# Kernel tuning notes

Measured on AMD Instinct MI355X. Metric: run time of the kernel, lower is better.

The kernel has to match this reference:

```python
import jax, jax.numpy as jnp
import numpy as np

B, N, H = 4, 512, 64
EDGE_IN = 2 * H + 4

def silu(x):
    return x * jax.nn.sigmoid(x)

def setup_inputs() -> dict:
    key = jax.random.key(0)
    ks = jax.random.split(key, 16)
    def w(k, fan_in, fan_out):
        return (jax.random.normal(k, (fan_in, fan_out), jnp.float32) / np.sqrt(fan_in)).astype(jnp.float32)
    return {
        "h":   jax.random.normal(ks[0], (B, N, H), jnp.float32),
        "pos": jax.random.normal(ks[1], (B, N, 2), jnp.float32),
        "vel": jax.random.normal(ks[2], (B, N, 2), jnp.float32),
        # edge_mlp: Linear(2H+4,H) SiLU Linear(H,H) SiLU
        "ew1": w(ks[3], EDGE_IN, H), "eb1": jnp.zeros((H,), jnp.float32),
        "ew2": w(ks[4], H, H),       "eb2": jnp.zeros((H,), jnp.float32),
        # force_mlp: Linear(H,H) SiLU Linear(H,1)
        "fw1": w(ks[5], H, H),       "fb1": jnp.zeros((H,), jnp.float32),
        "fw2": w(ks[6], H, 1),       "fb2": jnp.zeros((1,), jnp.float32),
        # node_mlp: Linear(2H,H) SiLU Linear(H,H)
        "nw1": w(ks[7], 2 * H, H),   "nb1": jnp.zeros((H,), jnp.float32),
        "nw2": w(ks[8], H, H),       "nb2": jnp.zeros((H,), jnp.float32),
    }

def reference(h, pos, vel, ew1, eb1, ew2, eb2, fw1, fb1, fw2, fb2, nw1, nb1, nw2, nb2):
    b, n, hd = h.shape
    # rel_pos[b,i,j] = pos[b,j] - pos[b,i]  (torch: pos.unsqueeze(1) - pos.unsqueeze(2))
    rel_pos = pos[:, None, :, :] - pos[:, :, None, :]                # (B,N,N,2)
    dist_sq = jnp.sum(rel_pos ** 2, axis=-1, keepdims=True)         # (B,N,N,1)
    dist = jnp.sqrt(dist_sq + 1e-8)
    normal = rel_pos / dist                                          # (B,N,N,2)
    speed_sq = jnp.sum(vel ** 2, axis=-1, keepdims=True)             # (B,N,1)
    rel_vel = vel[:, None, :, :] - vel[:, :, None, :]                # (B,N,N,2)
    approach = jnp.sum(rel_vel * normal, axis=-1, keepdims=True)     # (B,N,N,1)
    h_i = jnp.broadcast_to(h[:, :, None, :], (b, n, n, hd))
    h_j = jnp.broadcast_to(h[:, None, :, :], (b, n, n, hd))
    sp_i = jnp.broadcast_to(speed_sq[:, :, None, :], (b, n, n, 1))
    sp_j = jnp.broadcast_to(speed_sq[:, None, :, :], (b, n, n, 1))
    edge_feat = jnp.concatenate([h_i, h_j, dist_sq, sp_i, sp_j, approach], axis=-1)  # (B,N,N,2H+4)
    m_ij = silu(silu(edge_feat @ ew1 + eb1) @ ew2 + eb2)             # (B,N,N,H)
    force_weight = silu(m_ij @ fw1 + fb1) @ fw2 + fb2                # (B,N,N,1)
    force_ij = force_weight * normal                                 # (B,N,N,2)
    mask = (1.0 - jnp.eye(n, dtype=h.dtype))[None, :, :, None]       # zero self-edges
    force = jnp.sum(force_ij * mask, axis=2)                         # (B,N,2)
    m_agg = jnp.sum(m_ij * mask, axis=2)                             # (B,N,H)
    h_new = silu(jnp.concatenate([h, m_agg], axis=-1) @ nw1 + nb1) @ nw2 + nb2  # (B,N,H)
    return (h_new, force)
```

## Files before the change

### kernel.cpp

```cpp
#include <hip/hip_runtime.h>
#include <hip/hip_bf16.h>
#include <stdint.h>

#define NB 4
#define NN 512
#define NH 64

typedef __attribute__((ext_vector_type(4))) float f32x4;
typedef __attribute__((ext_vector_type(8))) short short8;

__device__ __forceinline__ unsigned short bf16b(float f){
  union { float f; uint32_t u; } c; c.f = f;
  uint32_t u = c.u;
  u += 0x7fffu + ((u >> 16) & 1u);
  return (unsigned short)(u >> 16);
}
__device__ __forceinline__ uint32_t pk2(float lo, float hi){
  uint32_t d;
  asm("v_cvt_pk_bf16_f32 %0, %1, %2" : "=v"(d) : "v"(lo), "v"(hi));
  return d;
}
__device__ __forceinline__ float silu(float x){
  float e = __expf(-x);
  return x * __builtin_amdgcn_rcpf(1.0f + e);
}

__launch_bounds__(256)
__global__ void k_precompute(const float* __restrict__ h,
                             const float* __restrict__ vel,
                             const float* __restrict__ ew1,
                             const float* __restrict__ eb1,
                             const float* __restrict__ ew2,
                             const float* __restrict__ fw1,
                             float* __restrict__ wa, float* __restrict__ wc,
                             unsigned short* __restrict__ wef,
                             unsigned short* __restrict__ wff){
  const int tid = threadIdx.x;
  if (blockIdx.x >= 512){
    const int idx = (blockIdx.x - 512) * 256 + tid;
    const int mat = idx >> 12;
    const int r = idx & 4095;
    const int e2 = r & 7;
    const int lane = (r >> 3) & 63;
    const int mtkk = r >> 9;
    const int kk = mtkk >> 2, mt = mtkk & 3;
    const int krow = kk*32 + (lane >> 4)*8 + e2;
    const int dr = lane & 15;
    const int col_nat  = mt*16 + dr;
    const int col_perm = 32*(mt>>1) + 8*(dr>>2) + 4*(mt&1) + (dr&3);
    if (mat) wff[r] = bf16b(fw1[krow*NH + col_nat]);
    else     wef[r] = bf16b(ew2[krow*NH + col_perm]);
    return;
  }
  const int row = blockIdx.x * 4 + (tid >> 6);
  const int t = tid & 63;
  const float* hr = h + row * NH;
  const float vx = vel[row*2], vy = vel[row*2+1];
  const float sp = vx*vx + vy*vy;
  float aa = eb1[t] + sp * ew1[129*NH + t];
  float cc =          sp * ew1[130*NH + t];
  #pragma unroll 8
  for (int k = 0; k < NH; ++k){
    float hk = hr[k];
    aa += hk * ew1[k*NH + t];
    cc += hk * ew1[(NH + k)*NH + t];
  }
  wa[row*NH + t] = aa;
  wc[row*NH + t] = cc;
}

__launch_bounds__(256)
__global__ void k_edges(const float* __restrict__ pos,
                        const float* __restrict__ vel,
                        const float* __restrict__ wa,
                        const float* __restrict__ wc,
                        const float* __restrict__ ew1,
                        const float* __restrict__ eb2,
                        const float* __restrict__ fb1,
                        const float* __restrict__ fw2,
                        const float* __restrict__ fb2,
                        const unsigned short* __restrict__ wef,
                        const unsigned short* __restrict__ wff,
                        float* __restrict__ wmagg,
                        float* __restrict__ outF){
  const int row = blockIdx.x;
  const int b = row >> 9;
  const int i = row & (NN - 1);
  const int tid = threadIdx.x;
  const int l = tid & 63;
  const int w = tid >> 6;
  const int e = l & 15;
  const int g = l >> 4;
  const int bN = b * NN;

  __shared__ alignas(16) float seb2[64];
  __shared__ alignas(16) float sfb1[64];
  __shared__ alignas(16) float sfw2[64];
  if (tid < 64){
    seb2[tid] = eb2[tid];
    sfb1[tid] = fb1[tid];
    sfw2[tid] = fw2[tid];
  }

  const float pix = pos[row*2], piy = pos[row*2+1];
  const float vix = vel[row*2], viy = vel[row*2+1];
  const float fb2s = fb2[0];

  const float* arow = wa + row * NH;
  const f32x4 af0a = *(const f32x4*)(arow + 8*g);
  const f32x4 af0b = *(const f32x4*)(arow + 8*g + 4);
  const f32x4 af1a = *(const f32x4*)(arow + 32 + 8*g);
  const f32x4 af1b = *(const f32x4*)(arow + 32 + 8*g + 4);
  const float* wD = ew1 + 128*NH;
  const f32x4 d0a = *(const f32x4*)(wD + 8*g);
  const f32x4 d0b = *(const f32x4*)(wD + 8*g + 4);
  const f32x4 d1a = *(const f32x4*)(wD + 32 + 8*g);
  const f32x4 d1b = *(const f32x4*)(wD + 32 + 8*g + 4);
  const float* wP = ew1 + 131*NH;
  const f32x4 p0a = *(const f32x4*)(wP + 8*g);
  const f32x4 p0b = *(const f32x4*)(wP + 8*g + 4);
  const f32x4 p1a = *(const f32x4*)(wP + 32 + 8*g);
  const f32x4 p1b = *(const f32x4*)(wP + 32 + 8*g + 4);

  short8 aw[2][4], fw[2][4];
  #pragma unroll
  for (int kk = 0; kk < 2; ++kk){
    #pragma unroll
    for (int mt = 0; mt < 4; ++mt){
      aw[kk][mt] = *(const short8*)(wef + ((kk*4 + mt)*64 + l)*8);
      fw[kk][mt] = *(const short8*)(wff + ((kk*4 + mt)*64 + l)*8);
    }
  }

  f32x4 magg[4];
  #pragma unroll
  for (int mt = 0; mt < 4; ++mt) magg[mt] = (f32x4){0.f,0.f,0.f,0.f};
  float fx = 0.f, fy = 0.f;

  __syncthreads();

  for (int it = 0; it < 8; ++it){
    const int jbase = (w + 4*it) * 16;
    const int j = jbase + e;
    const float2 pj = *(const float2*)(pos + (bN + j)*2);
    const float2 vj = *(const float2*)(vel + (bN + j)*2);
    const float rx = pj.x - pix, ry = pj.y - piy;
    const float ds = rx*rx + ry*ry;
    const float inv = __builtin_amdgcn_rsqf(ds + 1e-8f);
    const float nx = rx*inv, ny = ry*inv;
    const float ap = (vj.x - vix)*nx + (vj.y - viy)*ny;
    const float maskv = (j != i) ? 1.0f : 0.0f;

    const float* crow = wc + (bN + j)*NH;
    const f32x4 c0a = *(const f32x4*)(crow + 8*g);
    const f32x4 c0b = *(const f32x4*)(crow + 8*g + 4);
    const f32x4 c1a = *(const f32x4*)(crow + 32 + 8*g);
    const f32x4 c1b = *(const f32x4*)(crow + 32 + 8*g + 4);

    short8 bx[2];
    {
      union { uint32_t u[4]; short8 s; } cv;
      float s0 = silu(af0a.x + c0a.x + ds*d0a.x + ap*p0a.x);
      float s1 = silu(af0a.y + c0a.y + ds*d0a.y + ap*p0a.y);
      float s2 = silu(af0a.z + c0a.z + ds*d0a.z + ap*p0a.z);
      float s3 = silu(af0a.w + c0a.w + ds*d0a.w + ap*p0a.w);
      cv.u[0] = pk2(s0, s1); cv.u[1] = pk2(s2, s3);
      float s4 = silu(af0b.x + c0b.x + ds*d0b.x + ap*p0b.x);
      float s5 = silu(af0b.y + c0b.y + ds*d0b.y + ap*p0b.y);
      float s6 = silu(af0b.z + c0b.z + ds*d0b.z + ap*p0b.z);
      float s7 = silu(af0b.w + c0b.w + ds*d0b.w + ap*p0b.w);
      cv.u[2] = pk2(s4, s5); cv.u[3] = pk2(s6, s7);
      bx[0] = cv.s;
    }
    {
      union { uint32_t u[4]; short8 s; } cv;
      float s0 = silu(af1a.x + c1a.x + ds*d1a.x + ap*p1a.x);
      float s1 = silu(af1a.y + c1a.y + ds*d1a.y + ap*p1a.y);
      float s2 = silu(af1a.z + c1a.z + ds*d1a.z + ap*p1a.z);
      float s3 = silu(af1a.w + c1a.w + ds*d1a.w + ap*p1a.w);
      cv.u[0] = pk2(s0, s1); cv.u[1] = pk2(s2, s3);
      float s4 = silu(af1b.x + c1b.x + ds*d1b.x + ap*p1b.x);
      float s5 = silu(af1b.y + c1b.y + ds*d1b.y + ap*p1b.y);
      float s6 = silu(af1b.z + c1b.z + ds*d1b.z + ap*p1b.z);
      float s7 = silu(af1b.w + c1b.w + ds*d1b.w + ap*p1b.w);
      cv.u[2] = pk2(s4, s5); cv.u[3] = pk2(s6, s7);
      bx[1] = cv.s;
    }

    f32x4 accm[4];
    #pragma unroll
    for (int mt = 0; mt < 4; ++mt){
      accm[mt] = *(const f32x4*)(seb2 + 32*(mt>>1) + 8*g + 4*(mt&1));
      accm[mt] = __builtin_amdgcn_mfma_f32_16x16x32_bf16(aw[0][mt], bx[0], accm[mt], 0, 0, 0);
      accm[mt] = __builtin_amdgcn_mfma_f32_16x16x32_bf16(aw[1][mt], bx[1], accm[mt], 0, 0, 0);
    }

    uint32_t pkm[4][2];
    #pragma unroll
    for (int mt = 0; mt < 4; ++mt){
      float m0 = silu(accm[mt].x);
      float m1 = silu(accm[mt].y);
      float m2 = silu(accm[mt].z);
      float m3 = silu(accm[mt].w);
      magg[mt].x += maskv * m0;
      magg[mt].y += maskv * m1;
      magg[mt].z += maskv * m2;
      magg[mt].w += maskv * m3;
      pkm[mt][0] = pk2(m0, m1);
      pkm[mt][1] = pk2(m2, m3);
    }

    short8 bm[2];
    #pragma unroll
    for (int kk = 0; kk < 2; ++kk){
      union { uint32_t u[4]; short8 s; } cv;
      cv.u[0] = pkm[2*kk][0];
      cv.u[1] = pkm[2*kk][1];
      cv.u[2] = pkm[2*kk+1][0];
      cv.u[3] = pkm[2*kk+1][1];
      bm[kk] = cv.s;
    }

    float p = 0.f;
    #pragma unroll
    for (int mt = 0; mt < 4; ++mt){
      f32x4 acc2 = *(const f32x4*)(sfb1 + mt*16 + 4*g);
      acc2 = __builtin_amdgcn_mfma_f32_16x16x32_bf16(fw[0][mt], bm[0], acc2, 0, 0, 0);
      acc2 = __builtin_amdgcn_mfma_f32_16x16x32_bf16(fw[1][mt], bm[1], acc2, 0, 0, 0);
      const f32x4 f2v = *(const f32x4*)(sfw2 + mt*16 + 4*g);
      p += silu(acc2.x) * f2v.x;
      p += silu(acc2.y) * f2v.y;
      p += silu(acc2.z) * f2v.z;
      p += silu(acc2.w) * f2v.w;
    }
    p += __shfl_xor(p, 16);
    p += __shfl_xor(p, 32);
    const float fwt = p + fb2s;
    fx += maskv * fwt * nx;
    fy += maskv * fwt * ny;
  }

  __shared__ float smagg[4][64];
  __shared__ float sforce[4][2];

  #pragma unroll
  for (int mt = 0; mt < 4; ++mt){
    #pragma unroll
    for (int r = 0; r < 4; ++r){
      float v = magg[mt][r];
      v += __shfl_xor(v, 1);
      v += __shfl_xor(v, 2);
      v += __shfl_xor(v, 4);
      v += __shfl_xor(v, 8);
      if (e == 0) smagg[w][32*(mt>>1) + 8*g + 4*(mt&1) + r] = v;
    }
  }
  fx += __shfl_xor(fx, 1); fx += __shfl_xor(fx, 2); fx += __shfl_xor(fx, 4); fx += __shfl_xor(fx, 8);
  fy += __shfl_xor(fy, 1); fy += __shfl_xor(fy, 2); fy += __shfl_xor(fy, 4); fy += __shfl_xor(fy, 8);
  if (l == 0){ sforce[w][0] = fx; sforce[w][1] = fy; }
  __syncthreads();

  if (tid < 64)
    wmagg[row*NH + tid] = smagg[0][tid] + smagg[1][tid] + smagg[2][tid] + smagg[3][tid];
  if (tid == 0){
    outF[row*2]     = sforce[0][0] + sforce[1][0] + sforce[2][0] + sforce[3][0];
    outF[row*2 + 1] = sforce[0][1] + sforce[1][1] + sforce[2][1] + sforce[3][1];
  }
}

__launch_bounds__(256)
__global__ void k_node(const float* __restrict__ h,
                       const float* __restrict__ wmagg,
                       const float* __restrict__ nw1,
                       const float* __restrict__ nb1,
                       const float* __restrict__ nw2,
                       const float* __restrict__ nb2,
                       float* __restrict__ outH){
  const int tid = threadIdx.x;
  const int r = tid >> 6;
  const int row = blockIdx.x * 4 + r;
  const int t = tid & 63;
  __shared__ float t1[4][64];
  const float* hr = h + row * NH;
  const float* mr = wmagg + row * NH;
  float acc = nb1[t];
  #pragma unroll 8
  for (int k = 0; k < NH; ++k) acc += hr[k] * nw1[k*NH + t];
  #pragma unroll 8
  for (int k = 0; k < NH; ++k) acc += mr[k] * nw1[(NH + k)*NH + t];
  t1[r][t] = silu(acc);
  __syncthreads();
  float o = nb2[t];
  #pragma unroll 8
  for (int k = 0; k < NH; ++k) o += t1[r][k] * nw2[k*NH + t];
  outH[row*NH + t] = o;
}

extern "C" void kernel_launch(void* const* d_in, const int* in_sizes, int n_in,
                              void* d_out, int out_size, void* d_ws, size_t ws_size,
                              hipStream_t stream){
  const float* h   = (const float*)d_in[0];
  const float* pos = (const float*)d_in[1];
  const float* vel = (const float*)d_in[2];
  const float* ew1 = (const float*)d_in[3];
  const float* eb1 = (const float*)d_in[4];
  const float* ew2 = (const float*)d_in[5];
  const float* eb2 = (const float*)d_in[6];
  const float* fw1 = (const float*)d_in[7];
  const float* fb1 = (const float*)d_in[8];
  const float* fw2 = (const float*)d_in[9];
  const float* fb2 = (const float*)d_in[10];
  const float* nw1 = (const float*)d_in[11];
  const float* nb1 = (const float*)d_in[12];
  const float* nw2 = (const float*)d_in[13];
  const float* nb2 = (const float*)d_in[14];
  float* out = (float*)d_out;

  float* wa    = (float*)d_ws;
  float* wc    = wa + NB*NN*NH;
  float* wmagg = wc + NB*NN*NH;
  unsigned short* wef = (unsigned short*)(wmagg + NB*NN*NH);
  unsigned short* wff = wef + 4096;

  k_precompute<<<dim3(544), dim3(256), 0, stream>>>(h, vel, ew1, eb1, ew2, fw1,
                                                    wa, wc, wef, wff);
  k_edges<<<dim3(NB*NN), dim3(256), 0, stream>>>(pos, vel, wa, wc, ew1, eb2, fb1, fw2, fb2,
                                                 wef, wff, wmagg, out + NB*NN*NH);
  k_node<<<dim3(512), dim3(256), 0, stream>>>(h, wmagg, nw1, nb1, nw2, nb2, out);
}
```

Measured before the change: 173.6 us.

## Fuse node MLP into edge kernel and use packed f32x2 SiLU math

Removes the separate node-MLP kernel by running it as a tail in each edge block: the block reduces m_agg in LDS, then one wavefront computes the two node linear layers and writes h_new directly. This drops a launch and the workspace round-trip for m_agg. SiLU and the accumulations are also rewritten with two-wide float vectors so the compiler can emit packed FP32 instructions. The fused tail runs serially on one wave per block with uncoalesced weight reads, which lengthens each of the 2048 blocks.

Result: no change. 175.3 us (+1.0%).

```diff
diff --git a/kernel.cpp b/kernel.cpp
--- a/kernel.cpp
+++ b/kernel.cpp
@@ -7,6 +7,7 @@
 #define NH 64
 
 typedef __attribute__((ext_vector_type(4))) float f32x4;
+typedef __attribute__((ext_vector_type(2))) float f32x2;
 typedef __attribute__((ext_vector_type(8))) short short8;
 
 __device__ __forceinline__ unsigned short bf16b(float f){
@@ -23,6 +24,12 @@
 __device__ __forceinline__ float silu(float x){
   float e = __expf(-x);
   return x * __builtin_amdgcn_rcpf(1.0f + e);
+}
+__device__ __forceinline__ f32x2 silu2(f32x2 x){
+  f32x2 e = { __expf(-x.x), __expf(-x.y) };
+  f32x2 den = e + 1.0f;
+  f32x2 r = { __builtin_amdgcn_rcpf(den.x), __builtin_amdgcn_rcpf(den.y) };
+  return x * r;
 }
 
 __launch_bounds__(256)
@@ -70,7 +77,8 @@
 }
 
 __launch_bounds__(256)
-__global__ void k_edges(const float* __restrict__ pos,
+__global__ void k_edges(const float* __restrict__ h,
+                        const float* __restrict__ pos,
                         const float* __restrict__ vel,
                         const float* __restrict__ wa,
                         const float* __restrict__ wc,
@@ -81,7 +89,11 @@
                         const float* __restrict__ fb2,
                         const unsigned short* __restrict__ wef,
                         const unsigned short* __restrict__ wff,
-                        float* __restrict__ wmagg,
+                        const float* __restrict__ nw1,
+                        const float* __restrict__ nb1,
+                        const float* __restrict__ nw2,
+                        const float* __restrict__ nb2,
+                        float* __restrict__ outH,
                         float* __restrict__ outF){
   const int row = blockIdx.x;
   const int b = row >> 9;
@@ -132,9 +144,12 @@
     }
   }
 
-  f32x4 magg[4];
+  f32x2 magg01[4], magg23[4];
   #pragma unroll
-  for (int mt = 0; mt < 4; ++mt) magg[mt] = (f32x4){0.f,0.f,0.f,0.f};
+  for (int mt = 0; mt < 4; ++mt){
+    magg01[mt] = (f32x2){0.f, 0.f};
+    magg23[mt] = (f32x2){0.f, 0.f};
+  }
   float fx = 0.f, fy = 0.f;
 
   __syncthreads();
@@ -150,6 +165,9 @@
     const float nx = rx*inv, ny = ry*inv;
     const float ap = (vj.x - vix)*nx + (vj.y - viy)*ny;
     const float maskv = (j != i) ? 1.0f : 0.0f;
+    const f32x2 ds2 = {ds, ds};
+    const f32x2 ap2 = {ap, ap};
+    const f32x2 mask2 = {maskv, maskv};
 
     const float* crow = wc + (bN + j)*NH;
     const f32x4 c0a = *(const f32x4*)(crow + 8*g);
@@ -160,30 +178,22 @@
     short8 bx[2];
     {
       union { uint32_t u[4]; short8 s; } cv;
-      float s0 = silu(af0a.x + c0a.x + ds*d0a.x + ap*p0a.x);
-      float s1 = silu(af0a.y + c0a.y + ds*d0a.y + ap*p0a.y);
-      float s2 = silu(af0a.z + c0a.z + ds*d0a.z + ap*p0a.z);
-      float s3 = silu(af0a.w + c0a.w + ds*d0a.w + ap*p0a.w);
-      cv.u[0] = pk2(s0, s1); cv.u[1] = pk2(s2, s3);
-      float s4 = silu(af0b.x + c0b.x + ds*d0b.x + ap*p0b.x);
-      float s5 = silu(af0b.y + c0b.y + ds*d0b.y + ap*p0b.y);
-      float s6 = silu(af0b.z + c0b.z + ds*d0b.z + ap*p0b.z);
-      float s7 = silu(af0b.w + c0b.w + ds*d0b.w + ap*p0b.w);
-      cv.u[2] = pk2(s4, s5); cv.u[3] = pk2(s6, s7);
+      f32x2 s01 = silu2(af0a.xy + c0a.xy + d0a.xy*ds2 + p0a.xy*ap2);
+      f32x2 s23 = silu2(af0a.zw + c0a.zw + d0a.zw*ds2 + p0a.zw*ap2);
+      cv.u[0] = pk2(s01.x, s01.y); cv.u[1] = pk2(s23.x, s23.y);
+      f32x2 s45 = silu2(af0b.xy + c0b.xy + d0b.xy*ds2 + p0b.xy*ap2);
+      f32x2 s67 = silu2(af0b.zw + c0b.zw + d0b.zw*ds2 + p0b.zw*ap2);
+      cv.u[2] = pk2(s45.x, s45.y); cv.u[3] = pk2(s67.x, s67.y);
       bx[0] = cv.s;
     }
     {
       union { uint32_t u[4]; short8 s; } cv;
-      float s0 = silu(af1a.x + c1a.x + ds*d1a.x + ap*p1a.x);
-      float s1 = silu(af1a.y + c1a.y + ds*d1a.y + ap*p1a.y);
-      float s2 = silu(af1a.z + c1a.z + ds*d1a.z + ap*p1a.z);
-      float s3 = silu(af1a.w + c1a.w + ds*d1a.w + ap*p1a.w);
-      cv.u[0] = pk2(s0, s1); cv.u[1] = pk2(s2, s3);
-      float s4 = silu(af1b.x + c1b.x + ds*d1b.x + ap*p1b.x);
-      float s5 = silu(af1b.y + c1b.y + ds*d1b.y + ap*p1b.y);
-      float s6 = silu(af1b.z + c1b.z + ds*d1b.z + ap*p1b.z);
-      float s7 = silu(af1b.w + c1b.w + ds*d1b.w + ap*p1b.w);
-      cv.u[2] = pk2(s4, s5); cv.u[3] = pk2(s6, s7);
+      f32x2 s01 = silu2(af1a.xy + c1a.xy + d1a.xy*ds2 + p1a.xy*ap2);
+      f32x2 s23 = silu2(af1a.zw + c1a.zw + d1a.zw*ds2 + p1a.zw*ap2);
+      cv.u[0] = pk2(s01.x, s01.y); cv.u[1] = pk2(s23.x, s23.y);
+      f32x2 s45 = silu2(af1b.xy + c1b.xy + d1b.xy*ds2 + p1b.xy*ap2);
+      f32x2 s67 = silu2(af1b.zw + c1b.zw + d1b.zw*ds2 + p1b.zw*ap2);
+      cv.u[2] = pk2(s45.x, s45.y); cv.u[3] = pk2(s67.x, s67.y);
       bx[1] = cv.s;
     }
 
@@ -198,16 +208,12 @@
     uint32_t pkm[4][2];
     #pragma unroll
     for (int mt = 0; mt < 4; ++mt){
-      float m0 = silu(accm[mt].x);
-      float m1 = silu(accm[mt].y);
-      float m2 = silu(accm[mt].z);
-      float m3 = silu(accm[mt].w);
-      magg[mt].x += maskv * m0;
-      magg[mt].y += maskv * m1;
-      magg[mt].z += maskv * m2;
-      magg[mt].w += maskv * m3;
-      pkm[mt][0] = pk2(m0, m1);
-      pkm[mt][1] = pk2(m2, m3);
+      f32x2 m01 = silu2(accm[mt].xy);
+      f32x2 m23 = silu2(accm[mt].zw);
+      magg01[mt] = magg01[mt] + m01 * mask2;
+      magg23[mt] = magg23[mt] + m23 * mask2;
+      pkm[mt][0] = pk2(m01.x, m01.y);
+      pkm[mt][1] = pk2(m23.x, m23.y);
     }
 
     short8 bm[2];
@@ -221,18 +227,17 @@
       bm[kk] = cv.s;
     }
 
-    float p = 0.f;
+    f32x2 pacc = {0.f, 0.f};
     #pragma unroll
     for (int mt = 0; mt < 4; ++mt){
       f32x4 acc2 = *(const f32x4*)(sfb1 + mt*16 + 4*g);
       acc2 = __builtin_amdgcn_mfma_f32_16x16x32_bf16(fw[0][mt], bm[0], acc2, 0, 0, 0);
       acc2 = __builtin_amdgcn_mfma_f32_16x16x32_bf16(fw[1][mt], bm[1], acc2, 0, 0, 0);
       const f32x4 f2v = *(const f32x4*)(sfw2 + mt*16 + 4*g);
-      p += silu(acc2.x) * f2v.x;
-      p += silu(acc2.y) * f2v.y;
-      p += silu(acc2.z) * f2v.z;
-      p += silu(acc2.w) * f2v.w;
-    }
+      pacc = pacc + silu2(acc2.xy) * f2v.xy;
+      pacc = pacc + silu2(acc2.zw) * f2v.zw;
+    }
+    float p = pacc.x + pacc.y;
     p += __shfl_xor(p, 16);
     p += __shfl_xor(p, 32);
     const float fwt = p + fb2s;
@@ -247,7 +252,8 @@
   for (int mt = 0; mt < 4; ++mt){
     #pragma unroll
     for (int r = 0; r < 4; ++r){
-      float v = magg[mt][r];
+      float v = (r < 2) ? ((r & 1) ? magg01[mt].y : magg01[mt].x)
+                        : ((r & 1) ? magg23[mt].y : magg23[mt].x);
       v += __shfl_xor(v, 1);
       v += __shfl_xor(v, 2);
       v += __shfl_xor(v, 4);
@@ -260,40 +266,33 @@
   if (l == 0){ sforce[w][0] = fx; sforce[w][1] = fy; }
   __syncthreads();
 
-  if (tid < 64)
-    wmagg[row*NH + tid] = smagg[0][tid] + smagg[1][tid] + smagg[2][tid] + smagg[3][tid];
+  if (tid < 64){
+    const int t = tid;
+    smagg[0][t] = smagg[0][t] + smagg[1][t] + smagg[2][t] + smagg[3][t];
+  }
   if (tid == 0){
     outF[row*2]     = sforce[0][0] + sforce[1][0] + sforce[2][0] + sforce[3][0];
     outF[row*2 + 1] = sforce[0][1] + sforce[1][1] + sforce[2][1] + sforce[3][1];
   }
-}
-
-__launch_bounds__(256)
-__global__ void k_node(const float* __restrict__ h,
-                       const float* __restrict__ wmagg,
-                       const float* __restrict__ nw1,
-                       const float* __restrict__ nb1,
-                       const float* __restrict__ nw2,
-                       const float* __restrict__ nb2,
-                       float* __restrict__ outH){
-  const int tid = threadIdx.x;
-  const int r = tid >> 6;
-  const int row = blockIdx.x * 4 + r;
-  const int t = tid & 63;
-  __shared__ float t1[4][64];
-  const float* hr = h + row * NH;
-  const float* mr = wmagg + row * NH;
-  float acc = nb1[t];
-  #pragma unroll 8
-  for (int k = 0; k < NH; ++k) acc += hr[k] * nw1[k*NH + t];
-  #pragma unroll 8
-  for (int k = 0; k < NH; ++k) acc += mr[k] * nw1[(NH + k)*NH + t];
-  t1[r][t] = silu(acc);
   __syncthreads();
-  float o = nb2[t];
-  #pragma unroll 8
-  for (int k = 0; k < NH; ++k) o += t1[r][k] * nw2[k*NH + t];
-  outH[row*NH + t] = o;
+  if (tid < 64){
+    const int t = tid;
+    const float* hr = h + row * NH;
+    float acc = nb1[t];
+    #pragma unroll 8
+    for (int k = 0; k < NH; ++k) acc += hr[k] * nw1[k*NH + t];
+    #pragma unroll 8
+    for (int k = 0; k < NH; ++k) acc += smagg[0][k] * nw1[(NH + k)*NH + t];
+    smagg[1][t] = silu(acc);
+  }
+  __syncthreads();
+  if (tid < 64){
+    const int t = tid;
+    float o = nb2[t];
+    #pragma unroll 8
+    for (int k = 0; k < NH; ++k) o += smagg[1][k] * nw2[k*NH + t];
+    outH[row*NH + t] = o;
+  }
 }
 
 extern "C" void kernel_launch(void* const* d_in, const int* in_sizes, int n_in,
@@ -318,13 +317,12 @@
 
   float* wa    = (float*)d_ws;
   float* wc    = wa + NB*NN*NH;
-  float* wmagg = wc + NB*NN*NH;
-  unsigned short* wef = (unsigned short*)(wmagg + NB*NN*NH);
+  unsigned short* wef = (unsigned short*)(wc + NB*NN*NH);
   unsigned short* wff = wef + 4096;
 
   k_precompute<<<dim3(544), dim3(256), 0, stream>>>(h, vel, ew1, eb1, ew2, fw1,
                                                     wa, wc, wef, wff);
-  k_edges<<<dim3(NB*NN), dim3(256), 0, stream>>>(pos, vel, wa, wc, ew1, eb2, fb1, fw2, fb2,
-                                                 wef, wff, wmagg, out + NB*NN*NH);
-  k_node<<<dim3(512), dim3(256), 0, stream>>>(h, wmagg, nw1, nb1, nw2, nb2, out);
-}
+  k_edges<<<dim3(NB*NN), dim3(256), 0, stream>>>(h, pos, vel, wa, wc, ew1, eb2, fb1, fw2, fb2,
+                                                 wef, wff, nw1, nb1, nw2, nb2,
+                                                 out, out + NB*NN*NH);
+}
```
